# Kernel tuning notes

Hardware: AMD Instinct MI355X
Metric: run time of the kernel (lower is better)

Reference implementation:

```python
import jax, jax.numpy as jnp
import numpy as np

B, LQ, LK, H = 4, 512, 512, 256


def setup_inputs() -> dict:
    key = jax.random.key(0)
    ks = jax.random.split(key, 8)
    s = 1.0 / np.sqrt(H)  # torch Linear init scale
    return {
        "query": jax.random.normal(ks[0], (B, LQ, H), dtype=jnp.float32),
        "values": jax.random.normal(ks[1], (B, LK, H), dtype=jnp.float32),
        "Wq": jax.random.uniform(ks[2], (H, H), jnp.float32, -s, s),
        "bq": jax.random.uniform(ks[3], (H,), jnp.float32, -s, s),
        "Wk": jax.random.uniform(ks[4], (H, H), jnp.float32, -s, s),
        "bk": jax.random.uniform(ks[5], (H,), jnp.float32, -s, s),
        "We": jax.random.uniform(ks[6], (H,), jnp.float32, -s, s),
        "be": jax.random.uniform(ks[7], (1,), jnp.float32, -s, s),
    }


def reference(query, values, Wq, bq, Wk, bk, We, be):
    # Linear projections (torch: x @ W.T + b)
    q = jnp.einsum("bqh,oh->bqo", query, Wq) + bq      # (B, Lq, H)
    k = jnp.einsum("bkh,oh->bko", values, Wk) + bk     # (B, Lk, H)
    # Additive attention energy: (B, Lq, Lk, H) broadcast add + tanh
    energy = jnp.tanh(q[:, :, None, :] + k[:, None, :, :])
    # energy_layer: Linear(H -> 1), squeeze -> scores (B, Lq, Lk)
    scores = jnp.einsum("bqkh,h->bqk", energy, We) + be[0]
    attention = jax.nn.softmax(scores, axis=-1)         # (B, Lq, Lk)
    context = jnp.einsum("bqk,bkh->bqh", attention, values)  # (B, Lq, H)
    return context, attention
```

## Files before the change

### kernel.cpp

```cpp
#include <hip/hip_runtime.h>


#define SCALE2 2.8853900817779268f

#if defined(__has_builtin)
#if __has_builtin(__builtin_amdgcn_exp2f)
#define FEXP2(x) __builtin_amdgcn_exp2f(x)
#endif
#if __has_builtin(__builtin_amdgcn_rcpf)
#define FRCP(x) __builtin_amdgcn_rcpf(x)
#endif
#endif
#ifndef FEXP2
#define FEXP2(x) exp2f(x)
#endif
#ifndef FRCP
#define FRCP(x) (1.0f/(x))
#endif

typedef float f32x2 __attribute__((ext_vector_type(2)));

static __device__ __forceinline__ f32x2 pk2(float lo, float hi) {
  f32x2 r; r.x = lo; r.y = hi; return r;
}

static __device__ __forceinline__ void pk_quad_step(
    const f32x2 qp, const f32x2 kv01, const f32x2 kv23, const float w,
    f32x2 acc[4])
{
  const f32x2 one2 = pk2(1.0f, 1.0f);
  const f32x2 k0 = __builtin_shufflevector(kv01, kv01, 0, 0);
  const f32x2 k1 = __builtin_shufflevector(kv01, kv01, 1, 1);
  const f32x2 k2 = __builtin_shufflevector(kv23, kv23, 0, 0);
  const f32x2 k3 = __builtin_shufflevector(kv23, kv23, 1, 1);
  f32x2 x0 = __builtin_elementwise_fma(qp, k0, one2);
  f32x2 x1 = __builtin_elementwise_fma(qp, k1, one2);
  f32x2 x2 = __builtin_elementwise_fma(qp, k2, one2);
  f32x2 x3 = __builtin_elementwise_fma(qp, k3, one2);
  f32x2 p01 = x0 * x1, p23 = x2 * x3, P = p01 * p23;
  f32x2 rr; rr.x = FRCP(P.x); rr.y = FRCP(P.y);
  f32x2 wr = rr * w;
  f32x2 sw = wr * p23, uw = wr * p01;
  acc[0] = __builtin_elementwise_fma(sw, x1, acc[0]);
  acc[1] = __builtin_elementwise_fma(sw, x0, acc[1]);
  acc[2] = __builtin_elementwise_fma(uw, x3, acc[2]);
  acc[3] = __builtin_elementwise_fma(uw, x2, acc[3]);
}

__global__ __launch_bounds__(512) void proj_kernel(
    const float* __restrict__ Q, const float* __restrict__ V,
    const float* __restrict__ Wq, const float* __restrict__ bq,
    const float* __restrict__ Wk, const float* __restrict__ bk,
    float* __restrict__ EqT, float* __restrict__ EkT)
{
  const int n0 = blockIdx.x * 64;
  const int o0 = blockIdx.y * 64;
  const bool isK = (blockIdx.z == 1);
  const float* X    = isK ? V  : Q;
  const float* W    = isK ? Wk : Wq;
  const float* bias = isK ? bk : bq;
  const int t  = threadIdx.x;
  const int tx = t & 15;
  const int ty = t >> 4;
  __shared__ float Xst[32][68];
  __shared__ float Wst[32][68];
  float acc[2][4] = {};
  const int sr = t >> 3, sc = (t & 7) << 2;
  float4 xv = *(const float4*)(X + (size_t)(n0 + sr) * 256 + sc);
  float4 wv = *(const float4*)(W + (size_t)(o0 + sr) * 256 + sc);
  for (int h0 = 0; h0 < 256; h0 += 32) {
    __syncthreads();
    Xst[sc  ][sr] = xv.x; Xst[sc+1][sr] = xv.y; Xst[sc+2][sr] = xv.z; Xst[sc+3][sr] = xv.w;
    Wst[sc  ][sr] = wv.x; Wst[sc+1][sr] = wv.y; Wst[sc+2][sr] = wv.z; Wst[sc+3][sr] = wv.w;
    __syncthreads();
    if (h0 < 224) {
      xv = *(const float4*)(X + (size_t)(n0 + sr) * 256 + h0 + 32 + sc);
      wv = *(const float4*)(W + (size_t)(o0 + sr) * 256 + h0 + 32 + sc);
    }
#pragma unroll 8
    for (int hh = 0; hh < 32; ++hh) {
      float2 a  = *(const float2*)&Xst[hh][ty*2];
      float4 bb = *(const float4*)&Wst[hh][tx*4];
      acc[0][0] = fmaf(a.x, bb.x, acc[0][0]); acc[0][1] = fmaf(a.x, bb.y, acc[0][1]);
      acc[0][2] = fmaf(a.x, bb.z, acc[0][2]); acc[0][3] = fmaf(a.x, bb.w, acc[0][3]);
      acc[1][0] = fmaf(a.y, bb.x, acc[1][0]); acc[1][1] = fmaf(a.y, bb.y, acc[1][1]);
      acc[1][2] = fmaf(a.y, bb.z, acc[1][2]); acc[1][3] = fmaf(a.y, bb.w, acc[1][3]);
    }
  }
  const float4 bv = *(const float4*)(bias + o0 + tx*4);
  float e[2][4];
#pragma unroll
  for (int i = 0; i < 2; ++i) {
    e[i][0] = FEXP2(SCALE2 * (acc[i][0] + bv.x));
    e[i][1] = FEXP2(SCALE2 * (acc[i][1] + bv.y));
    e[i][2] = FEXP2(SCALE2 * (acc[i][2] + bv.z));
    e[i][3] = FEXP2(SCALE2 * (acc[i][3] + bv.w));
  }
  float* outT = isK ? EkT : EqT;
  const int b  = n0 >> 9;
  const int nl = (n0 & 511) + ty*2;
#pragma unroll
  for (int j = 0; j < 4; ++j) {
    float2 st = {e[0][j], e[1][j]};
    *(float2*)(outT + (size_t)b*131072 + (size_t)(o0 + tx*4 + j)*512 + nl) = st;
  }
}

__global__ __launch_bounds__(256) void scores_kernel(
    const float* __restrict__ EqT, const float* __restrict__ EkT,
    const float* __restrict__ We, float* __restrict__ pt)
{
  const int flat = blockIdx.x;
  const int kt = flat & 3;
  const int qt = (flat >> 2) & 7;
  const int z  = flat >> 5;
  const int b = z >> 2, half = z & 3;
  const int h0 = half * 64;
  const int t  = threadIdx.x;
  const int qr = t >> 4;
  const int kr = t & 15;

  __shared__ float4 qs4[2][32][16];
  __shared__ float4 ks4[2][32][32];

  const float* eqb = EqT + (size_t)b*131072 + (size_t)h0*512 + qt*64;
  const float* ekb = EkT + (size_t)b*131072 + (size_t)h0*512 + kt*128;

  const int rs = t >> 3;
  const int sq = (t & 7) * 2;
  const int sk = (t & 7) * 4;

  float4 aq0 = *(const float4*)(eqb + (size_t)rs*512 + (sq  )*4);
  float4 aq1 = *(const float4*)(eqb + (size_t)rs*512 + (sq+1)*4);
  float4 ak[4];
#pragma unroll
  for (int j = 0; j < 4; ++j)
    ak[j] = *(const float4*)(ekb + (size_t)rs*512 + (sk+j)*4);
  qs4[0][rs][sq] = aq0; qs4[0][rs][sq+1] = aq1;
#pragma unroll
  for (int j = 0; j < 4; ++j) ks4[0][rs][sk+j] = ak[j];

  float4 bq0 = *(const float4*)(eqb + (size_t)(32+rs)*512 + (sq  )*4);
  float4 bq1 = *(const float4*)(eqb + (size_t)(32+rs)*512 + (sq+1)*4);
  float4 bk[4];
#pragma unroll
  for (int j = 0; j < 4; ++j)
    bk[j] = *(const float4*)(ekb + (size_t)(32+rs)*512 + (sk+j)*4);

  __syncthreads();

  f32x2 acc[2][2][4];
#pragma unroll
  for (int p = 0; p < 2; ++p)
#pragma unroll
    for (int c = 0; c < 2; ++c)
#pragma unroll
      for (int j = 0; j < 4; ++j) acc[p][c][j] = pk2(0.f, 0.f);

#pragma unroll 4
  for (int hh = 0; hh < 32; ++hh) {
    const float w = We[h0 + hh];
    const float4 qv  = qs4[0][hh][qr];
    const float4 kv0 = ks4[0][hh][kr];
    const float4 kv1 = ks4[0][hh][kr + 16];
    const f32x2 qlo = pk2(qv.x, qv.y), qhi = pk2(qv.z, qv.w);
    const f32x2 k0a = pk2(kv0.x, kv0.y), k0b = pk2(kv0.z, kv0.w);
    const f32x2 k1a = pk2(kv1.x, kv1.y), k1b = pk2(kv1.z, kv1.w);
    pk_quad_step(qlo, k0a, k0b, w, acc[0][0]);
    pk_quad_step(qlo, k1a, k1b, w, acc[0][1]);
    pk_quad_step(qhi, k0a, k0b, w, acc[1][0]);
    pk_quad_step(qhi, k1a, k1b, w, acc[1][1]);
  }

  qs4[1][rs][sq] = bq0; qs4[1][rs][sq+1] = bq1;
#pragma unroll
  for (int j = 0; j < 4; ++j) ks4[1][rs][sk+j] = bk[j];
  __syncthreads();

#pragma unroll 4
  for (int hh = 0; hh < 32; ++hh) {
    const float w = We[h0 + 32 + hh];
    const float4 qv  = qs4[1][hh][qr];
    const float4 kv0 = ks4[1][hh][kr];
    const float4 kv1 = ks4[1][hh][kr + 16];
    const f32x2 qlo = pk2(qv.x, qv.y), qhi = pk2(qv.z, qv.w);
    const f32x2 k0a = pk2(kv0.x, kv0.y), k0b = pk2(kv0.z, kv0.w);
    const f32x2 k1a = pk2(kv1.x, kv1.y), k1b = pk2(kv1.z, kv1.w);
    pk_quad_step(qlo, k0a, k0b, w, acc[0][0]);
    pk_quad_step(qlo, k1a, k1b, w, acc[0][1]);
    pk_quad_step(qhi, k0a, k0b, w, acc[1][0]);
    pk_quad_step(qhi, k1a, k1b, w, acc[1][1]);
  }

  float* sout = pt + (size_t)half*1048576
                   + (size_t)(b*512 + qt*64 + qr*4)*512 + kt*128 + kr*4;
#pragma unroll
  for (int p = 0; p < 2; ++p) {
#pragma unroll
    for (int s = 0; s < 2; ++s) {
      const int i = p*2 + s;
      float4 s0, s1;
      if (s == 0) {
        s0 = (float4){acc[p][0][0].x, acc[p][0][1].x, acc[p][0][2].x, acc[p][0][3].x};
        s1 = (float4){acc[p][1][0].x, acc[p][1][1].x, acc[p][1][2].x, acc[p][1][3].x};
      } else {
        s0 = (float4){acc[p][0][0].y, acc[p][0][1].y, acc[p][0][2].y, acc[p][0][3].y};
        s1 = (float4){acc[p][1][0].y, acc[p][1][1].y, acc[p][1][2].y, acc[p][1][3].y};
      }
      *(float4*)(sout + (size_t)i*512) = s0;
      *(float4*)(sout + (size_t)i*512 + 64) = s1;
    }
  }
}

__global__ __launch_bounds__(512) void ctx_kernel(
    const float* __restrict__ values, const float* __restrict__ pt,
    float* __restrict__ attn, float* __restrict__ ctx)
{
  const int t    = threadIdx.x;
  const int row0 = blockIdx.x * 8;
  const int b    = row0 >> 9;
  __shared__ float ts[8][512];
  __shared__ float red[8][8][256];

#pragma unroll
  for (int rep = 0; rep < 2; ++rep) {
    int idx = rep*512 + t;
    int r = idx >> 7, c = (idx & 127) << 2;
    size_t off = (size_t)(row0 + r)*512 + c;
    float4 v0 = *(const float4*)(pt + off);
    float4 v1 = *(const float4*)(pt + 1048576 + off);
    float4 v2 = *(const float4*)(pt + 2097152 + off);
    float4 v3 = *(const float4*)(pt + 3145728 + off);
    float4 s = {v0.x+v1.x+v2.x+v3.x, v0.y+v1.y+v2.y+v3.y,
                v0.z+v1.z+v2.z+v3.z, v0.w+v1.w+v2.w+v3.w};
    *(float4*)&ts[r][c] = s;
  }
  __syncthreads();

  const int w = t >> 6, j = t & 63;
  {
    float v[8];
    float mn = 1e30f;
#pragma unroll
    for (int i = 0; i < 8; ++i) { v[i] = ts[w][j + 64*i]; mn = fminf(mn, v[i]); }
#pragma unroll
    for (int off = 32; off > 0; off >>= 1) mn = fminf(mn, __shfl_xor(mn, off, 64));
    float sum = 0.f;
#pragma unroll
    for (int i = 0; i < 8; ++i) { v[i] = FEXP2((mn - v[i]) * SCALE2); sum += v[i]; }
#pragma unroll
    for (int off = 32; off > 0; off >>= 1) sum += __shfl_xor(sum, off, 64);
    const float inv = 1.0f / sum;
    float* gp = attn + (size_t)(row0 + w) * 512 + j;
#pragma unroll
    for (int i = 0; i < 8; ++i) {
      float p = v[i] * inv;
      ts[w][j + 64*i] = p;
      gp[64*i] = p;
    }
  }
  __syncthreads();

  const int h4 = j << 2;
  const int wk0 = w * 64;
  const float* vwb = values + (size_t)b*131072 + (size_t)wk0*256 + h4;
  float4 acc[8];
#pragma unroll
  for (int r = 0; r < 8; ++r) acc[r] = (float4){0,0,0,0};

  float4 cv[4], nv[4];
#pragma unroll
  for (int jj = 0; jj < 4; ++jj) cv[jj] = *(const float4*)(vwb + (size_t)jj*256);

  for (int kq = 0; kq < 16; ++kq) {
    if (kq < 15) {
#pragma unroll
      for (int jj = 0; jj < 4; ++jj)
        nv[jj] = *(const float4*)(vwb + (size_t)((kq+1)*4 + jj)*256);
    }
    float4 a[8];
#pragma unroll
    for (int r = 0; r < 8; ++r) a[r] = *(const float4*)&ts[r][wk0 + kq*4];
#pragma unroll
    for (int jj = 0; jj < 4; ++jj) {
      float4 v4 = cv[jj];
#pragma unroll
      for (int r = 0; r < 8; ++r) {
        float ar = (jj == 0) ? a[r].x : (jj == 1) ? a[r].y : (jj == 2) ? a[r].z : a[r].w;
        acc[r].x = fmaf(ar, v4.x, acc[r].x);
        acc[r].y = fmaf(ar, v4.y, acc[r].y);
        acc[r].z = fmaf(ar, v4.z, acc[r].z);
        acc[r].w = fmaf(ar, v4.w, acc[r].w);
      }
    }
#pragma unroll
    for (int jj = 0; jj < 4; ++jj) cv[jj] = nv[jj];
  }

#pragma unroll
  for (int r = 0; r < 8; ++r) *(float4*)&red[w][r][h4] = acc[r];
  __syncthreads();
  {
    const int rr = t >> 6;
    const int hh4 = (t & 63) << 2;
    float4 s = *(const float4*)&red[0][rr][hh4];
#pragma unroll
    for (int ww = 1; ww < 8; ++ww) {
      float4 p = *(const float4*)&red[ww][rr][hh4];
      s.x += p.x; s.y += p.y; s.z += p.z; s.w += p.w;
    }
    *(float4*)(ctx + (size_t)(row0 + rr)*256 + hh4) = s;
  }
}

extern "C" void kernel_launch(void* const* d_in, const int* in_sizes, int n_in,
                              void* d_out, int out_size, void* d_ws, size_t ws_size,
                              hipStream_t stream)
{
  const float* query  = (const float*)d_in[0];
  const float* values = (const float*)d_in[1];
  const float* Wq     = (const float*)d_in[2];
  const float* bq     = (const float*)d_in[3];
  const float* Wk     = (const float*)d_in[4];
  const float* bk     = (const float*)d_in[5];
  const float* We     = (const float*)d_in[6];

  float* ctx  = (float*)d_out;
  float* attn = ctx + 4*512*256;
  float* EqT  = (float*)d_ws;
  float* EkT  = EqT + 524288;
  float* pt   = EkT + 524288;

  proj_kernel  <<<dim3(32, 4, 2), 512, 0, stream>>>(query, values, Wq, bq, Wk, bk, EqT, EkT);
  scores_kernel<<<512, 256, 0, stream>>>(EqT, EkT, We, pt);
  ctx_kernel   <<<256, 512, 0, stream>>>(values, pt, attn, ctx);
}
```

Baseline: 60.45 us.

## Split hidden dim into two partials with 512-thread blocks and pipelined chunk loads

The scores kernel now splits the hidden dimension into 2 partial sums of 128 instead of 4 of 64. It uses 512-thread blocks in which each thread computes a 2x8 tile instead of 4x8, and double-buffers four 32-wide hidden chunks, prefetching the next chunk into registers during compute. This halves the partial-score traffic written by scores and read back by ctx_kernel, which now sums two partials instead of four. In exchange there are fewer blocks (256), less register reuse per thread, and more barriers per block.

```diff
diff --git a/kernel.cpp b/kernel.cpp
--- a/kernel.cpp
+++ b/kernel.cpp
@@ -106,7 +106,7 @@
   }
 }
 
-__global__ __launch_bounds__(256) void scores_kernel(
+__global__ __launch_bounds__(512) void scores_kernel(
     const float* __restrict__ EqT, const float* __restrict__ EkT,
     const float* __restrict__ We, float* __restrict__ pt)
 {
@@ -114,103 +114,99 @@
   const int kt = flat & 3;
   const int qt = (flat >> 2) & 7;
   const int z  = flat >> 5;
-  const int b = z >> 2, half = z & 3;
-  const int h0 = half * 64;
+  const int b = z >> 1, half = z & 1;
+  const int h0 = half * 128;
   const int t  = threadIdx.x;
   const int qr = t >> 4;
   const int kr = t & 15;
 
-  __shared__ float4 qs4[2][32][16];
+  __shared__ float  qs [2][32][64];
   __shared__ float4 ks4[2][32][32];
 
   const float* eqb = EqT + (size_t)b*131072 + (size_t)h0*512 + qt*64;
   const float* ekb = EkT + (size_t)b*131072 + (size_t)h0*512 + kt*128;
 
-  const int rs = t >> 3;
-  const int sq = (t & 7) * 2;
-  const int sk = (t & 7) * 4;
-
-  float4 aq0 = *(const float4*)(eqb + (size_t)rs*512 + (sq  )*4);
-  float4 aq1 = *(const float4*)(eqb + (size_t)rs*512 + (sq+1)*4);
-  float4 ak[4];
-#pragma unroll
-  for (int j = 0; j < 4; ++j)
-    ak[j] = *(const float4*)(ekb + (size_t)rs*512 + (sk+j)*4);
-  qs4[0][rs][sq] = aq0; qs4[0][rs][sq+1] = aq1;
-#pragma unroll
-  for (int j = 0; j < 4; ++j) ks4[0][rs][sk+j] = ak[j];
-
-  float4 bq0 = *(const float4*)(eqb + (size_t)(32+rs)*512 + (sq  )*4);
-  float4 bq1 = *(const float4*)(eqb + (size_t)(32+rs)*512 + (sq+1)*4);
-  float4 bk[4];
-#pragma unroll
-  for (int j = 0; j < 4; ++j)
-    bk[j] = *(const float4*)(ekb + (size_t)(32+rs)*512 + (sk+j)*4);
-
+  const int rq = t >> 4, cq = (t & 15) << 2;
+
+  float4 aq[2];
+  float4 ak[2][2];
+
+  aq[0] = *(const float4*)(eqb + (size_t)rq*512 + cq);
+#pragma unroll
+  for (int rep = 0; rep < 2; ++rep) {
+    int idx = rep*512 + t;
+    int r = idx >> 5, c = idx & 31;
+    ak[0][rep] = *(const float4*)(ekb + (size_t)r*512 + c*4);
+  }
+  *(float4*)&qs[0][rq][cq] = aq[0];
+#pragma unroll
+  for (int rep = 0; rep < 2; ++rep) {
+    int idx = rep*512 + t;
+    int r = idx >> 5, c = idx & 31;
+    ks4[0][r][c] = ak[0][rep];
+  }
+  aq[1] = *(const float4*)(eqb + (size_t)(32 + rq)*512 + cq);
+#pragma unroll
+  for (int rep = 0; rep < 2; ++rep) {
+    int idx = rep*512 + t;
+    int r = idx >> 5, c = idx & 31;
+    ak[1][rep] = *(const float4*)(ekb + (size_t)(32 + r)*512 + c*4);
+  }
   __syncthreads();
 
-  f32x2 acc[2][2][4];
-#pragma unroll
-  for (int p = 0; p < 2; ++p)
-#pragma unroll
-    for (int c = 0; c < 2; ++c)
-#pragma unroll
-      for (int j = 0; j < 4; ++j) acc[p][c][j] = pk2(0.f, 0.f);
-
+  f32x2 acc[2][4];
+#pragma unroll
+  for (int c = 0; c < 2; ++c)
+#pragma unroll
+    for (int j = 0; j < 4; ++j) acc[c][j] = pk2(0.f, 0.f);
+
+#pragma unroll
+  for (int ch = 0; ch < 4; ++ch) {
+    const int buf = ch & 1;
 #pragma unroll 4
-  for (int hh = 0; hh < 32; ++hh) {
-    const float w = We[h0 + hh];
-    const float4 qv  = qs4[0][hh][qr];
-    const float4 kv0 = ks4[0][hh][kr];
-    const float4 kv1 = ks4[0][hh][kr + 16];
-    const f32x2 qlo = pk2(qv.x, qv.y), qhi = pk2(qv.z, qv.w);
-    const f32x2 k0a = pk2(kv0.x, kv0.y), k0b = pk2(kv0.z, kv0.w);
-    const f32x2 k1a = pk2(kv1.x, kv1.y), k1b = pk2(kv1.z, kv1.w);
-    pk_quad_step(qlo, k0a, k0b, w, acc[0][0]);
-    pk_quad_step(qlo, k1a, k1b, w, acc[0][1]);
-    pk_quad_step(qhi, k0a, k0b, w, acc[1][0]);
-    pk_quad_step(qhi, k1a, k1b, w, acc[1][1]);
-  }
-
-  qs4[1][rs][sq] = bq0; qs4[1][rs][sq+1] = bq1;
-#pragma unroll
-  for (int j = 0; j < 4; ++j) ks4[1][rs][sk+j] = bk[j];
-  __syncthreads();
-
-#pragma unroll 4
-  for (int hh = 0; hh < 32; ++hh) {
-    const float w = We[h0 + 32 + hh];
-    const float4 qv  = qs4[1][hh][qr];
-    const float4 kv0 = ks4[1][hh][kr];
-    const float4 kv1 = ks4[1][hh][kr + 16];
-    const f32x2 qlo = pk2(qv.x, qv.y), qhi = pk2(qv.z, qv.w);
-    const f32x2 k0a = pk2(kv0.x, kv0.y), k0b = pk2(kv0.z, kv0.w);
-    const f32x2 k1a = pk2(kv1.x, kv1.y), k1b = pk2(kv1.z, kv1.w);
-    pk_quad_step(qlo, k0a, k0b, w, acc[0][0]);
-    pk_quad_step(qlo, k1a, k1b, w, acc[0][1]);
-    pk_quad_step(qhi, k0a, k0b, w, acc[1][0]);
-    pk_quad_step(qhi, k1a, k1b, w, acc[1][1]);
+    for (int hh = 0; hh < 32; ++hh) {
+      const float w = We[h0 + ch*32 + hh];
+      const f32x2 qp  = *(const f32x2*)&qs[buf][hh][qr*2];
+      const float4 kv0 = ks4[buf][hh][kr];
+      const float4 kv1 = ks4[buf][hh][kr + 16];
+      const f32x2 k0a = pk2(kv0.x, kv0.y), k0b = pk2(kv0.z, kv0.w);
+      const f32x2 k1a = pk2(kv1.x, kv1.y), k1b = pk2(kv1.z, kv1.w);
+      pk_quad_step(qp, k0a, k0b, w, acc[0]);
+      pk_quad_step(qp, k1a, k1b, w, acc[1]);
+    }
+    if (ch < 3) {
+      const int nset = (ch + 1) & 1;
+      *(float4*)&qs[buf ^ 1][rq][cq] = aq[nset];
+#pragma unroll
+      for (int rep = 0; rep < 2; ++rep) {
+        int idx = rep*512 + t;
+        int r = idx >> 5, c = idx & 31;
+        ks4[buf ^ 1][r][c] = ak[nset][rep];
+      }
+      if (ch < 2) {
+        const int lset = ch & 1;
+        aq[lset] = *(const float4*)(eqb + (size_t)((ch+2)*32 + rq)*512 + cq);
+#pragma unroll
+        for (int rep = 0; rep < 2; ++rep) {
+          int idx = rep*512 + t;
+          int r = idx >> 5, c = idx & 31;
+          ak[lset][rep] = *(const float4*)(ekb + (size_t)((ch+2)*32 + r)*512 + c*4);
+        }
+      }
+      __syncthreads();
+    }
   }
 
   float* sout = pt + (size_t)half*1048576
-                   + (size_t)(b*512 + qt*64 + qr*4)*512 + kt*128 + kr*4;
-#pragma unroll
-  for (int p = 0; p < 2; ++p) {
-#pragma unroll
-    for (int s = 0; s < 2; ++s) {
-      const int i = p*2 + s;
-      float4 s0, s1;
-      if (s == 0) {
-        s0 = (float4){acc[p][0][0].x, acc[p][0][1].x, acc[p][0][2].x, acc[p][0][3].x};
-        s1 = (float4){acc[p][1][0].x, acc[p][1][1].x, acc[p][1][2].x, acc[p][1][3].x};
-      } else {
-        s0 = (float4){acc[p][0][0].y, acc[p][0][1].y, acc[p][0][2].y, acc[p][0][3].y};
-        s1 = (float4){acc[p][1][0].y, acc[p][1][1].y, acc[p][1][2].y, acc[p][1][3].y};
-      }
-      *(float4*)(sout + (size_t)i*512) = s0;
-      *(float4*)(sout + (size_t)i*512 + 64) = s1;
-    }
-  }
+                   + (size_t)(b*512 + qt*64 + qr*2)*512 + kt*128 + kr*4;
+  float4 r0c0 = {acc[0][0].x, acc[0][1].x, acc[0][2].x, acc[0][3].x};
+  float4 r0c1 = {acc[1][0].x, acc[1][1].x, acc[1][2].x, acc[1][3].x};
+  float4 r1c0 = {acc[0][0].y, acc[0][1].y, acc[0][2].y, acc[0][3].y};
+  float4 r1c1 = {acc[1][0].y, acc[1][1].y, acc[1][2].y, acc[1][3].y};
+  *(float4*)(sout)            = r0c0;
+  *(float4*)(sout + 64)       = r0c1;
+  *(float4*)(sout + 512)      = r1c0;
+  *(float4*)(sout + 512 + 64) = r1c1;
 }
 
 __global__ __launch_bounds__(512) void ctx_kernel(
@@ -230,10 +226,7 @@
     size_t off = (size_t)(row0 + r)*512 + c;
     float4 v0 = *(const float4*)(pt + off);
     float4 v1 = *(const float4*)(pt + 1048576 + off);
-    float4 v2 = *(const float4*)(pt + 2097152 + off);
-    float4 v3 = *(const float4*)(pt + 3145728 + off);
-    float4 s = {v0.x+v1.x+v2.x+v3.x, v0.y+v1.y+v2.y+v3.y,
-                v0.z+v1.z+v2.z+v3.z, v0.w+v1.w+v2.w+v3.w};
+    float4 s = {v0.x+v1.x, v0.y+v1.y, v0.z+v1.z, v0.w+v1.w};
     *(float4*)&ts[r][c] = s;
   }
   __syncthreads();
@@ -333,6 +326,6 @@
   float* pt   = EkT + 524288;
 
   proj_kernel  <<<dim3(32, 4, 2), 512, 0, stream>>>(query, values, Wq, bq, Wk, bk, EqT, EkT);
-  scores_kernel<<<512, 256, 0, stream>>>(EqT, EkT, We, pt);
+  scores_kernel<<<256, 512, 0, stream>>>(EqT, EkT, We, pt);
   ctx_kernel   <<<256, 512, 0, stream>>>(values, pt, attn, ctx);
 }
```

New measurement: 62.06 us. +2.7%, slower.
